# Performance work log

Measured on AMD Instinct MI355X. Metric: run time of the kernel, lower is better.

## Reference

```python
import jax, jax.numpy as jnp
import numpy as np

# nqsystems=8 grouped sites, physical dim d=2^ncontraq=16,
# state bond r=64, layer (unitary MPO) bond rl=16, operator MPO bond ro=4,
# nlsystems=1 pre-contracted circuit layer.
NQ, R, D, RL, RO, NL = 8, 64, 16, 16, 4, 1


def setup_inputs() -> dict:
    key = jax.random.key(0)
    k1, k2, k3 = jax.random.split(key, 3)
    # scale so contractions stay O(1) numerically
    state = jax.random.normal(k1, (NQ, R, D, R), jnp.float32) / np.float32(np.sqrt(R * D))
    layer = jax.random.normal(k2, (NL, NQ, RL, D, D, RL), jnp.float32) / np.float32(np.sqrt(RL * D))
    operator = jax.random.normal(k3, (NQ, RO, D, D, RO), jnp.float32) / np.float32(np.sqrt(RO * D))
    return {"state": state, "layer": layer, "operator": operator}


def reference(state, layer, operator):
    """<psi| U^dagger O U |psi> contracted site-by-site along the TT chain.

    state:    [nq, r, d, r]        TT cores of |psi>
    layer:    [nl, nq, rl, d, d, rl]  TT-operator cores of the circuit layer (nl=1)
    operator: [nq, ro, d, d, ro]   TT-operator cores of the observable
    """
    r, rl, ro = state.shape[1], layer.shape[3], operator.shape[1]
    # open-boundary closure: boundary vectors = e0 on every bond
    env0 = jnp.zeros((r, rl, ro, rl, r), state.dtype).at[0, 0, 0, 0, 0].set(1.0)
    U = layer[0]  # nlsystems == 1

    def step(env, cores):
        S, Uq, Oq = cores
        # tt_dagger: conj + transpose physical indices (0,2,1,3)
        Ud = jnp.conj(Uq).transpose(0, 2, 1, 3)
        # env axes: a=bra-state bond, l=bra-layer bond, o=operator bond,
        #           m=ket-layer bond, b=ket-state bond
        t = jnp.einsum('alomb,aiA->lombiA', env, jnp.conj(S))   # bra state core
        t = jnp.einsum('lombiA,lijL->ombAjL', t, Ud)            # U^dagger core
        t = jnp.einsum('ombAjL,ojkO->mbALkO', t, Oq)            # observable core
        t = jnp.einsum('mbALkO,mksM->bALOsM', t, Uq)            # U core
        t = jnp.einsum('bALOsM,bsB->ALOMB', t, S)               # ket state core
        return t, None

    env, _ = jax.lax.scan(step, env0, (state, U, operator))
    return env[0, 0, 0, 0, 0]
```

## Files before the change

kernel.cpp:

```cpp
#include <hip/hip_runtime.h>


typedef __attribute__((ext_vector_type(8))) short bf16x8;
typedef __attribute__((ext_vector_type(8))) _Float16 f16x8;
typedef __attribute__((ext_vector_type(4))) float f32x4;
typedef __attribute__((ext_vector_type(4))) unsigned short us4;

static __device__ __forceinline__ unsigned short f2bf(float x) {
    union { float f; unsigned u; } a; a.f = x;
    return (unsigned short)((a.u + 0x7FFF + ((a.u >> 16) & 1)) >> 16);
}
static __device__ __forceinline__ float bf2f(unsigned short h) {
    union { unsigned u; float f; } a; a.u = (unsigned)h << 16; return a.f;
}
static __device__ __forceinline__ unsigned split2(float x) {
    unsigned short h = f2bf(x);
    unsigned short l = f2bf(x - bf2f(h));
    return (unsigned)h | ((unsigned)l << 16);
}
static __device__ __forceinline__ unsigned short f2h_bits(float x) {
    union { _Float16 h; unsigned short u; } c; c.h = (_Float16)x; return c.u;
}
static __device__ __forceinline__ float h2f_bits(unsigned short u) {
    union { unsigned short u; _Float16 h; } c; c.u = u; return (float)c.h;
}
static __device__ __forceinline__ void gl_lds16(const unsigned short* g,
                                                unsigned short* l) {
    __builtin_amdgcn_global_load_lds(
        (const __attribute__((address_space(1))) unsigned int*)g,
        (__attribute__((address_space(3))) unsigned int*)l, 16, 0, 0);
}

__global__ void write_diag_kernel(float* out, float v) {
    if (threadIdx.x == 0 && blockIdx.x == 0) out[0] = v;
}
__global__ void zero_out(float* o) {
    if (threadIdx.x == 0 && blockIdx.x == 0) o[0] = 0.0f;
}

__global__ void prep_apack(const float* __restrict__ layer,
                           unsigned short* __restrict__ Ap2,
                           unsigned short* __restrict__ Ap4) {
    int idx = blockIdx.x * 256 + threadIdx.x;
    int q = idx >> 13, k0 = (idx >> 10) & 7, mt = (idx >> 6) & 15, lane = idx & 63;
    int quad = lane >> 4, r = lane & 15;
    unsigned short h2[8], l2[8], h4[8], l4[8];
#pragma unroll
    for (int j = 0; j < 8; j++) {
        int k = k0 * 32 + quad * 8 + j;
        int m = mt * 16 + r;
        float v2 = layer[(size_t)q * 65536 +
                         (size_t)((((k >> 4) * 16 + (m >> 4)) * 16 + (k & 15)) * 16 + (m & 15))];
        float v4 = layer[(size_t)q * 65536 +
                         (size_t)((((k >> 4) * 16 + (k & 15)) * 16 + (m >> 4)) * 16 + (m & 15))];
        h2[j] = f2h_bits(v2); l2[j] = f2h_bits(v2 - h2f_bits(h2[j]));
        h4[j] = f2h_bits(v4); l4[j] = f2h_bits(v4 - h2f_bits(h4[j]));
    }
    size_t base = ((size_t)((q * 8 + k0) * 16 + mt) * 2) * 512 + lane * 8;
    *(us4*)(Ap2 + base)       = *(us4*)&h2[0];
    *(us4*)(Ap2 + base + 4)   = *(us4*)&h2[4];
    *(us4*)(Ap2 + base + 512) = *(us4*)&l2[0];
    *(us4*)(Ap2 + base + 516) = *(us4*)&l2[4];
    *(us4*)(Ap4 + base)       = *(us4*)&h4[0];
    *(us4*)(Ap4 + base + 4)   = *(us4*)&h4[4];
    *(us4*)(Ap4 + base + 512) = *(us4*)&l4[0];
    *(us4*)(Ap4 + base + 516) = *(us4*)&l4[4];
}

__global__ void prep_spack1(const float* __restrict__ state,
                            unsigned short* __restrict__ Sp1) {
    int idx = blockIdx.x * 256 + threadIdx.x;
    int q = idx >> 13, c = (idx >> 11) & 3, k0 = (idx >> 10) & 1,
        mt = (idx >> 6) & 15, lane = idx & 63;
    int quad = lane >> 4, lr = lane & 15;
    unsigned short h[8], l[8];
#pragma unroll
    for (int j = 0; j < 8; j++) {
        int k = k0 * 32 + quad * 8 + j;
        float v = state[(size_t)q * 65536 + (size_t)(k * 16 + mt) * 64 + c * 16 + lr];
        h[j] = f2bf(v); l[j] = f2bf(v - bf2f(h[j]));
    }
    size_t base = (size_t)(q * 4 + c) * 32768 + ((size_t)(k0 * 16 + mt) * 2) * 512 + lane * 8;
    *(us4*)(Sp1 + base)       = *(us4*)&h[0];
    *(us4*)(Sp1 + base + 4)   = *(us4*)&h[4];
    *(us4*)(Sp1 + base + 512) = *(us4*)&l[0];
    *(us4*)(Sp1 + base + 516) = *(us4*)&l[4];
}

__global__ void prep_spack5(const float* __restrict__ state,
                            unsigned short* __restrict__ Sp5) {
    int idx = blockIdx.x * 256 + threadIdx.x;
    int q = idx >> 13, k0 = (idx >> 8) & 31, mt = (idx >> 6) & 3, lane = idx & 63;
    int quad = lane >> 4, lr = lane & 15;
    unsigned short h[8], l[8];
#pragma unroll
    for (int j = 0; j < 8; j++) {
        int k = k0 * 32 + quad * 8 + j;
        int s = k >> 6, b = k & 63;
        float v = state[(size_t)q * 65536 + (size_t)(b * 16 + s) * 64 + mt * 16 + lr];
        h[j] = f2bf(v); l[j] = f2bf(v - bf2f(h[j]));
    }
    size_t base = (size_t)q * 131072 + ((size_t)(k0 * 4 + mt) * 2) * 512 + lane * 8;
    *(us4*)(Sp5 + base)       = *(us4*)&h[0];
    *(us4*)(Sp5 + base + 4)   = *(us4*)&h[4];
    *(us4*)(Sp5 + base + 512) = *(us4*)&l[0];
    *(us4*)(Sp5 + base + 516) = *(us4*)&l[4];
}

__global__ void prep_opack3(const float* __restrict__ oper,
                            unsigned short* __restrict__ Op3) {
    int idx = blockIdx.x * 256 + threadIdx.x;
    int q = idx >> 9, k0 = (idx >> 8) & 1, mt = (idx >> 6) & 3, lane = idx & 63;
    int quad = lane >> 4, lr = lane & 15;
    unsigned short h[8], l[8];
#pragma unroll
    for (int j = 0; j < 8; j++) {
        int k = k0 * 32 + quad * 8 + j;
        int m = mt * 16 + lr;
        float v = oper[(size_t)q * 4096 + (size_t)(k * 16 + (m & 15)) * 4 + (m >> 4)];
        h[j] = f2h_bits(v); l[j] = f2h_bits(v - h2f_bits(h[j]));
    }
    size_t base = (size_t)q * 8192 + ((size_t)(k0 * 4 + mt) * 2) * 512 + lane * 8;
    *(us4*)(Op3 + base)       = *(us4*)&h[0];
    *(us4*)(Op3 + base + 4)   = *(us4*)&h[4];
    *(us4*)(Op3 + base + 512) = *(us4*)&l[0];
    *(us4*)(Op3 + base + 516) = *(us4*)&l[4];
}

__global__ void env_split_k(const float* __restrict__ env, unsigned* __restrict__ envS) {
    int t = blockIdx.x * 256 + threadIdx.x;
    float4 v = ((const float4*)env)[t];
    uint4 o;
    o.x = split2(v.x); o.y = split2(v.y); o.z = split2(v.z); o.w = split2(v.w);
    ((uint4*)envS)[t] = o;
}

__global__ void s0_g2(const float* __restrict__ state, const float* __restrict__ layer,
                      float* __restrict__ g2) {
    int t = blockIdx.x * 256 + threadIdx.x;
    int A = t >> 8, j = (t >> 4) & 15, L = t & 15;
    float s = 0;
    for (int i = 0; i < 16; i++) s += state[i * 64 + A] * layer[(j * 16 + i) * 16 + L];
    g2[t] = s;
}
__global__ void s0_g3(const float* __restrict__ g2, const float* __restrict__ oper,
                      float* __restrict__ g3) {
    int t = blockIdx.x * 256 + threadIdx.x;
    int A = t >> 10, L = (t >> 6) & 15, k = (t >> 2) & 15, O = t & 3;
    float s = 0;
    for (int j = 0; j < 16; j++) s += g2[A * 256 + j * 16 + L] * oper[(j * 16 + k) * 4 + O];
    g3[t] = s;
}
__global__ void s0_g4(const float* __restrict__ g3, const float* __restrict__ layer,
                      float* __restrict__ g4) {
    int t = blockIdx.x * 256 + threadIdx.x;
    int A = t >> 14, L = (t >> 10) & 15, O = (t >> 8) & 3, sp = (t >> 4) & 15, M = t & 15;
    float s = 0;
    for (int k = 0; k < 16; k++)
        s += g3[A * 1024 + L * 64 + k * 4 + O] * layer[(k * 16 + sp) * 16 + M];
    g4[t] = s;
}
__global__ void s0_env(const float* __restrict__ g4, const float* __restrict__ state,
                       float* __restrict__ env) {
    int t = blockIdx.x * 256 + threadIdx.x;
    int A = t >> 16, L = (t >> 12) & 15, O = (t >> 10) & 3, M = (t >> 6) & 15, B = t & 63;
    float s = 0;
    for (int sp = 0; sp < 16; sp++)
        s += g4[A * 16384 + L * 1024 + O * 256 + sp * 16 + M] * state[sp * 64 + B];
    env[(size_t)(L * 64 + O * 16 + M) * 4096 + A * 64 + B] = s;
}

__global__ void s7_c1(const float* __restrict__ state, const float* __restrict__ layer,
                      float* __restrict__ c1) {
    int t = blockIdx.x * 256 + threadIdx.x;
    int l = t >> 10, a = (t >> 4) & 63, j = t & 15;
    float s = 0;
    for (int i = 0; i < 16; i++)
        s += state[7 * 65536 + (a * 16 + i) * 64] * layer[7 * 65536 + ((l * 16 + j) * 16 + i) * 16];
    c1[t] = s;
}
__global__ void s7_c2(const float* __restrict__ c1, const float* __restrict__ oper,
                      float* __restrict__ c2) {
    int t = blockIdx.x * 256 + threadIdx.x;
    int o = t >> 14, l = (t >> 10) & 15, a = (t >> 4) & 63, k = t & 15;
    float s = 0;
    for (int j = 0; j < 16; j++)
        s += c1[l * 1024 + a * 16 + j] * oper[7 * 4096 + ((o * 16 + j) * 16 + k) * 4];
    c2[t] = s;
}
__global__ void s7_c3(const float* __restrict__ c2, const float* __restrict__ layer,
                      float* __restrict__ c3) {
    int t = blockIdx.x * 256 + threadIdx.x;
    int m = t >> 16, o = (t >> 14) & 3, l = (t >> 10) & 15, a = (t >> 4) & 63, sp = t & 15;
    float s = 0;
    for (int k = 0; k < 16; k++)
        s += c2[o * 16384 + l * 1024 + a * 16 + k] *
             layer[7 * 65536 + ((m * 16 + k) * 16 + sp) * 16];
    c3[t] = s;
}
__global__ void prep_sv(const float* __restrict__ state, float* __restrict__ sv) {
    int t = blockIdx.x * 256 + threadIdx.x;
    sv[t] = state[7 * 65536 + t * 64];
}
__global__ __launch_bounds__(256) void s7_fused(const float* __restrict__ env,
                                                const float* __restrict__ c3,
                                                const float* __restrict__ sv,
                                                float* __restrict__ out) {
    __shared__ float c3s[1024], svs[1024], red[256];
    int t = threadIdx.x;
    int n0 = blockIdx.x * 64;
    int l = n0 >> 12, o = (n0 >> 10) & 3, m = (n0 >> 6) & 15;
    const float* c3b = c3 + m * 65536 + o * 16384 + l * 1024;
    const float* eb  = env + (size_t)blockIdx.x * 4096;
    for (int i = t; i < 1024; i += 256) { c3s[i] = c3b[i]; svs[i] = sv[i]; }
    __syncthreads();
    float s = 0;
    int b = t & 63, ag = t >> 6;
#pragma unroll
    for (int g = 0; g < 16; g++) {
        int a = ag * 16 + g;
        float e = eb[a * 64 + b];
        float w = 0;
#pragma unroll
        for (int sp = 0; sp < 16; sp++) w += c3s[a * 16 + sp] * svs[b * 16 + sp];
        s += e * w;
    }
    red[t] = s; __syncthreads();
    for (int off = 128; off; off >>= 1) { if (t < off) red[t] += red[t + off]; __syncthreads(); }
    if (t == 0) atomicAdd(out, red[0]);
}

__global__ __launch_bounds__(256) void gemm_g1(const unsigned* __restrict__ envS,
                                               const unsigned short* __restrict__ Sp1,
                                               unsigned short* __restrict__ t1,
                                               float scale) {
    __shared__ unsigned Bt[32 * 65];
    const int tid = threadIdx.x, lane = tid & 63, wave = tid >> 6;
    const int quad = lane >> 4, lr = lane & 15;
    const int cc = blockIdx.x >> 10, rid = blockIdx.x & 1023;
    const int l = rid >> 6, o = (rid >> 4) & 3, m2 = rid & 15;

    f32x4 acc[4][4];
#pragma unroll
    for (int i = 0; i < 4; i++)
#pragma unroll
        for (int j = 0; j < 4; j++)
#pragma unroll
            for (int r = 0; r < 4; r++) acc[i][j][r] = 0.0f;

    const unsigned* Bv = envS + (size_t)rid * 4096;
    const unsigned short* Sp1c = Sp1 + (size_t)cc * 32768;
    uint4 ur[2];
    auto load_tile = [&](int k0) {
        const uint4* src = (const uint4*)(Bv + k0 * 2048);
        ur[0] = src[tid];
        ur[1] = src[256 + tid];
    };
    auto store_tile = [&]() {
#pragma unroll
        for (int v = 0; v < 2; v++) {
            int e = v * 256 + tid;
            unsigned* p = &Bt[(e >> 4) * 65 + (e & 15) * 4];
            p[0] = ur[v].x; p[1] = ur[v].y; p[2] = ur[v].z; p[3] = ur[v].w;
        }
    };

    bf16x8 ahb[2][4], alb[2][4];
    auto loadA = [&](int k0, int buf) {
#pragma unroll
        for (int mt = 0; mt < 4; mt++) {
            int gmt = wave * 4 + mt;
            const unsigned short* ap = Sp1c + ((size_t)(k0 * 16 + gmt) * 2) * 512 + lane * 8;
            ahb[buf][mt] = *(const bf16x8*)ap;
            alb[buf][mt] = *(const bf16x8*)(ap + 512);
        }
    };

    load_tile(0);
    loadA(0, 0);
    store_tile();
#pragma unroll
    for (int k0 = 0; k0 < 2; k0++) {
        __syncthreads();
        if (k0 + 1 < 2) { load_tile(k0 + 1); loadA(k0 + 1, 1); }
#pragma unroll
        for (int nt = 0; nt < 4; nt++) {
            int nl = nt * 16 + lr;
            bf16x8 bh, bl;
#pragma unroll
            for (int j = 0; j < 8; j++) {
                unsigned u = Bt[(quad * 8 + j) * 65 + nl];
                bh[j] = (short)(u & 0xffffu);
                bl[j] = (short)(u >> 16);
            }
#pragma unroll
            for (int mt = 0; mt < 4; mt++) {
                acc[mt][nt] = __builtin_amdgcn_mfma_f32_16x16x32_bf16(ahb[k0][mt], bh, acc[mt][nt], 0, 0, 0);
                acc[mt][nt] = __builtin_amdgcn_mfma_f32_16x16x32_bf16(ahb[k0][mt], bl, acc[mt][nt], 0, 0, 0);
                acc[mt][nt] = __builtin_amdgcn_mfma_f32_16x16x32_bf16(alb[k0][mt], bh, acc[mt][nt], 0, 0, 0);
            }
        }
        __syncthreads();
        if (k0 + 1 < 2) store_tile();
    }

#pragma unroll
    for (int nt = 0; nt < 4; nt++) {
        int b = nt * 16 + lr;
#pragma unroll
        for (int r = 0; r < 4; r++) {
            int a4 = quad * 4 + r;
            us4 w;
#pragma unroll
            for (int mt = 0; mt < 4; mt++) w[mt] = f2h_bits(acc[mt][nt][r] * scale);
            size_t addr = (size_t)cc * 16777216 +
                          (size_t)(o * 256 + m2 * 16 + a4) * 16384 +
                          (size_t)(l * 2 + (wave >> 1)) * 512 + b * 8 + (wave & 1) * 4;
            *(us4*)(t1 + addr) = w;
        }
    }
}

__global__ __launch_bounds__(256) void gemm_g2(const unsigned short* __restrict__ Bp,
                                               const unsigned short* __restrict__ Ap,
                                               unsigned short* __restrict__ Co) {
    __shared__ __align__(16) unsigned short Bs[16384];
    const int tid = threadIdx.x, lane = tid & 63, wave = tid >> 6;
    const int quad = lane >> 4, lr = lane & 15;
    const int cc = blockIdx.x >> 10, rid = blockIdx.x & 1023;
    const int o = rid >> 8, m2 = (rid >> 4) & 15, a4 = rid & 15;
    const unsigned short* pb = Bp + (size_t)blockIdx.x * 16384;
    unsigned short* Cb = Co + (size_t)cc * 16777216;

#pragma unroll
    for (int i = 0; i < 8; i++)
        gl_lds16(pb + i * 2048 + tid * 8, Bs + i * 2048 + wave * 512);

    f32x4 acc[4][4];
#pragma unroll
    for (int i = 0; i < 4; i++)
#pragma unroll
        for (int j = 0; j < 4; j++)
#pragma unroll
            for (int r = 0; r < 4; r++) acc[i][j][r] = 0.0f;

    f16x8 ah[3][4];
    auto loadA = [&](int k0, int buf) {
#pragma unroll
        for (int mt = 0; mt < 4; mt++) {
            int gmt = wave * 4 + mt;
            ah[buf][mt] = *(const f16x8*)(Ap + ((size_t)(k0 * 16 + gmt) * 2) * 512 + lane * 8);
        }
    };
    loadA(0, 0);
    loadA(1, 1);

    asm volatile("s_waitcnt vmcnt(0)" ::: "memory");
    __syncthreads();

#pragma unroll
    for (int k0 = 0; k0 < 8; k0++) {
        if (k0 + 2 < 8) loadA(k0 + 2, (k0 + 2) % 3);
        f16x8 bfr[4];
#pragma unroll
        for (int nt = 0; nt < 4; nt++)
            bfr[nt] = *(const f16x8*)(Bs + (k0 * 4 + quad) * 512 + (nt * 16 + lr) * 8);
#pragma unroll
        for (int nt = 0; nt < 4; nt++)
#pragma unroll
            for (int mt = 0; mt < 4; mt++)
                acc[mt][nt] = __builtin_amdgcn_mfma_f32_16x16x32_f16(
                    ah[k0 % 3][mt], bfr[nt], acc[mt][nt], 0, 0, 0);
    }

#pragma unroll
    for (int nt = 0; nt < 4; nt++) {
        int b = nt * 16 + lr;
#pragma unroll
        for (int r = 0; r < 4; r++) {
            int L = quad * 4 + r;
            us4 w;
#pragma unroll
            for (int mt = 0; mt < 4; mt++) w[mt] = f2h_bits(acc[mt][nt][r]);
            size_t addr = (size_t)(L * 256 + m2 * 16 + a4) * 4096 +
                          (size_t)(o * 2 + (wave >> 1)) * 512 + b * 8 + (wave & 1) * 4;
            *(us4*)(Cb + addr) = w;
        }
    }
}

__global__ __launch_bounds__(256) void gemm_g45(const unsigned short* __restrict__ T2,
                                                const unsigned short* __restrict__ Op3q,
                                                const unsigned short* __restrict__ Ap4,
                                                const unsigned short* __restrict__ Sp5,
                                                float* __restrict__ env,
                                                unsigned* __restrict__ envSo,
                                                int A0, float inv, int wf32) {
    __shared__ __align__(16) unsigned short Bs[16384];
    __shared__ unsigned SL[4 * 16 * 68];
    const int tid = threadIdx.x, lane = tid & 63, wave = tid >> 6;
    const int quad = lane >> 4, lr = lane & 15;
    const int cc = blockIdx.x >> 10, rid = blockIdx.x & 1023;
    const int low = rid & 7, O2 = (rid >> 3) & 3, g = rid >> 5;
    const int panel = g * 8 + low;
    const int L = panel >> 4, a4 = panel & 15;
    const unsigned short* T2c = T2 + (size_t)cc * 16777216;
    const int b8 = (wave * 16 + lr) * 8;

    f16x8 ah[3][4];
    auto loadA = [&](int k0, int buf) {
#pragma unroll
        for (int mt = 0; mt < 4; mt++) {
            int gmt = wave * 4 + mt;
            ah[buf][mt] = *(const f16x8*)(Ap4 + ((size_t)(k0 * 16 + gmt) * 2) * 512 + lane * 8);
        }
    };
    loadA(0, 0);
    loadA(1, 1);

    {
        f16x8 oh0 = *(const f16x8*)(Op3q + (size_t)(O2 * 2) * 512 + lane * 8);
        f16x8 oh1 = *(const f16x8*)(Op3q + (size_t)((4 + O2) * 2) * 512 + lane * 8);
        f16x8 tb[3][2];
        auto loadT2 = [&](int m2, int buf) {
            const unsigned short* pp = T2c + (size_t)(L * 256 + m2 * 16 + a4) * 4096;
            tb[buf][0] = *(const f16x8*)(pp + (quad << 9) + b8);
            tb[buf][1] = *(const f16x8*)(pp + ((4 + quad) << 9) + b8);
        };
        loadT2(0, 0);
        loadT2(1, 1);
#pragma unroll
        for (int m2 = 0; m2 < 16; m2++) {
            if (m2 + 2 < 16) loadT2(m2 + 2, (m2 + 2) % 3);
            f32x4 a3;
            a3[0] = a3[1] = a3[2] = a3[3] = 0.0f;
            a3 = __builtin_amdgcn_mfma_f32_16x16x32_f16(oh0, tb[m2 % 3][0], a3, 0, 0, 0);
            a3 = __builtin_amdgcn_mfma_f32_16x16x32_f16(oh1, tb[m2 % 3][1], a3, 0, 0, 0);
            us4 w;
#pragma unroll
            for (int r = 0; r < 4; r++) w[r] = f2h_bits(a3[r]);
            *(us4*)(Bs + (m2 * 2 + (quad >> 1)) * 512 + b8 + (quad & 1) * 4) = w;
        }
    }
    __syncthreads();

    f32x4 acc[4][4];
#pragma unroll
    for (int i = 0; i < 4; i++)
#pragma unroll
        for (int j = 0; j < 4; j++)
#pragma unroll
            for (int r = 0; r < 4; r++) acc[i][j][r] = 0.0f;

#pragma unroll
    for (int k0 = 0; k0 < 8; k0++) {
        if (k0 + 2 < 8) loadA(k0 + 2, (k0 + 2) % 3);
        f16x8 bfr[4];
#pragma unroll
        for (int nt = 0; nt < 4; nt++)
            bfr[nt] = *(const f16x8*)(Bs + (k0 * 4 + quad) * 512 + (nt * 16 + lr) * 8);
#pragma unroll
        for (int nt = 0; nt < 4; nt++)
#pragma unroll
            for (int mt = 0; mt < 4; mt++)
                acc[mt][nt] = __builtin_amdgcn_mfma_f32_16x16x32_f16(
                    ah[k0 % 3][mt], bfr[nt], acc[mt][nt], 0, 0, 0);
    }

    unsigned* myslab = SL + wave * (16 * 68);
    f32x4 acc5[4];
#pragma unroll
    for (int nt = 0; nt < 4; nt++)
#pragma unroll
        for (int r = 0; r < 4; r++) acc5[nt][r] = 0.0f;

    bf16x8 s5h[2][4], s5l[2][4];
    auto loadS5 = [&](int step, int buf) {
        int kg = (wave * 4 + (step >> 1)) * 2 + (step & 1);
#pragma unroll
        for (int nt = 0; nt < 4; nt++) {
            const unsigned short* bp = Sp5 + ((size_t)(kg * 4 + nt) * 2) * 512 + lane * 8;
            s5h[buf][nt] = *(const bf16x8*)bp;
            s5l[buf][nt] = *(const bf16x8*)(bp + 512);
        }
    };
    loadS5(0, 0);

#pragma unroll
    for (int mtp = 0; mtp < 4; mtp++) {
#pragma unroll
        for (int nt = 0; nt < 4; nt++)
#pragma unroll
            for (int r = 0; r < 4; r++)
                myslab[(quad * 4 + r) * 68 + nt * 16 + lr] = split2(acc[mtp][nt][r]);
        asm volatile("s_waitcnt lgkmcnt(0)" ::: "memory");
#pragma unroll
        for (int h = 0; h < 2; h++) {
            const int step = mtp * 2 + h;
            const unsigned* sp = &myslab[lr * 68 + h * 32 + quad * 8];
            uint4 u0 = *(const uint4*)sp;
            uint4 u1 = *(const uint4*)(sp + 4);
            bf16x8 th, tl;
            th[0] = (short)(u0.x & 0xffff); tl[0] = (short)(u0.x >> 16);
            th[1] = (short)(u0.y & 0xffff); tl[1] = (short)(u0.y >> 16);
            th[2] = (short)(u0.z & 0xffff); tl[2] = (short)(u0.z >> 16);
            th[3] = (short)(u0.w & 0xffff); tl[3] = (short)(u0.w >> 16);
            th[4] = (short)(u1.x & 0xffff); tl[4] = (short)(u1.x >> 16);
            th[5] = (short)(u1.y & 0xffff); tl[5] = (short)(u1.y >> 16);
            th[6] = (short)(u1.z & 0xffff); tl[6] = (short)(u1.z >> 16);
            th[7] = (short)(u1.w & 0xffff); tl[7] = (short)(u1.w >> 16);
            if (step + 1 < 8) loadS5(step + 1, (step + 1) & 1);
#pragma unroll
            for (int nt = 0; nt < 4; nt++) {
                acc5[nt] = __builtin_amdgcn_mfma_f32_16x16x32_bf16(th, s5h[step & 1][nt], acc5[nt], 0, 0, 0);
                acc5[nt] = __builtin_amdgcn_mfma_f32_16x16x32_bf16(th, s5l[step & 1][nt], acc5[nt], 0, 0, 0);
                acc5[nt] = __builtin_amdgcn_mfma_f32_16x16x32_bf16(tl, s5h[step & 1][nt], acc5[nt], 0, 0, 0);
            }
        }
    }

    __syncthreads();
    float* red = (float*)SL;
#pragma unroll
    for (int nt = 0; nt < 4; nt++)
#pragma unroll
        for (int r = 0; r < 4; r++)
            red[wave * 1088 + (quad * 4 + r) * 68 + nt * 16 + lr] = acc5[nt][r];
    __syncthreads();
#pragma unroll
    for (int r = 0; r < 4; r++) {
        int M2 = quad * 4 + r, Bc = wave * 16 + lr;
        float v = red[M2 * 68 + Bc] + red[1088 + M2 * 68 + Bc] +
                  red[2176 + M2 * 68 + Bc] + red[3264 + M2 * 68 + Bc];
        float w = v * inv;
        size_t idx = (size_t)(L * 64 + O2 * 16 + M2) * 4096 + (A0 + cc * 16 + a4) * 64 + Bc;
        envSo[idx] = split2(w);
        if (wf32) env[idx] = w;
    }
}

extern "C" void kernel_launch(void* const* d_in, const int* in_sizes, int n_in,
                              void* d_out, int out_size, void* d_ws, size_t ws_size,
                              hipStream_t stream) {
    const float* state = (const float*)d_in[0];
    const float* layer = (const float*)d_in[1];
    const float* oper  = (const float*)d_in[2];
    float* out = (float*)d_out;

    const size_t need = 16777216ull * 4 + 33554432ull * 4 + 3ull * 4194304ull * 4 +
                        (4ull * 1048576ull + 65536ull) * 2ull + 4096ull;
    if (ws_size < need) {
        write_diag_kernel<<<1, 64, 0, stream>>>(out, (float)ws_size);
        return;
    }
    float* F    = (float*)d_ws;
    unsigned* P = (unsigned*)(F + 16777216);
    unsigned* envS0 = (unsigned*)(P + 33554432);
    float* envB = (float*)(envS0 + 4194304);
    unsigned* envS1 = (unsigned*)(envB + 4194304);
    unsigned short* Ap2 = (unsigned short*)(envS1 + 4194304);
    unsigned short* Ap4 = Ap2 + 1048576;
    unsigned short* Sp1 = Ap4 + 1048576;
    unsigned short* Sp5 = Sp1 + 1048576;
    unsigned short* Op3 = Sp5 + 1048576;
    float* sv = (float*)(Op3 + 65536);
    float* SCR = F;
    unsigned short* T1 = (unsigned short*)P;
    unsigned short* T2 = (unsigned short*)F;

    prep_apack<<<256, 256, 0, stream>>>(layer, Ap2, Ap4);
    prep_spack1<<<256, 256, 0, stream>>>(state, Sp1);
    prep_spack5<<<256, 256, 0, stream>>>(state, Sp5);
    prep_opack3<<<16, 256, 0, stream>>>(oper, Op3);
    prep_sv<<<4, 256, 0, stream>>>(state, sv);

    s0_g2<<<64, 256, 0, stream>>>(state, layer, SCR);
    s0_g3<<<256, 256, 0, stream>>>(SCR, oper, SCR + 16384);
    s0_g4<<<4096, 256, 0, stream>>>(SCR + 16384, layer, SCR + 81920);
    s0_env<<<16384, 256, 0, stream>>>(SCR + 81920, state, envB);
    env_split_k<<<4096, 256, 0, stream>>>(envB, envS1);

    for (int q = 1; q < 7; q++) {
        unsigned* einS  = (q & 1) ? envS1 : envS0;
        unsigned* eoutS = (q & 1) ? envS0 : envS1;
        float scl = (float)(1u << (16 + 2 * q));
        float inv = 1.0f / scl;
        int wf32 = (q == 6) ? 1 : 0;
        for (int p = 0; p < 2; p++) {
            gemm_g1<<<2048, 256, 0, stream>>>(
                einS, Sp1 + (size_t)(q * 4 + p * 2) * 32768, T1, scl);
            gemm_g2<<<2048, 256, 0, stream>>>(
                T1, Ap2 + (size_t)q * 131072, T2);
            gemm_g45<<<2048, 256, 0, stream>>>(
                T2, Op3 + (size_t)q * 8192, Ap4 + (size_t)q * 131072,
                Sp5 + (size_t)q * 131072, envB, eoutS, p * 32, inv, wf32);
        }
    }

    s7_c1<<<64, 256, 0, stream>>>(state, layer, SCR);
    s7_c2<<<256, 256, 0, stream>>>(SCR, oper, SCR + 16384);
    s7_c3<<<4096, 256, 0, stream>>>(SCR + 16384, layer, SCR + 81920);
    zero_out<<<1, 64, 0, stream>>>(out);
    s7_fused<<<1024, 256, 0, stream>>>(envB, SCR + 81920, sv, out);
}
```

Before: 1.444 ms.

## Fuse g45 of first half with g1 of second half, pack bf16 splits

Merges the gemm_g45 launch for the first half of each site step with the gemm_g1 launch for the second half into one interleaved grid, so the two independent phases share the GPU and one launch boundary is removed. The split of floats into hi/lo bf16 pairs now uses packed v_cvt_pk_bf16_f32 and v_perm instructions in place of scalar bit manipulation. The T2 prefetch depth in g45 goes from 2 to 4. The risks are T1 being overwritten while g2 still needs it (the ordering looks safe here because g2 finished before the fused launch), higher register pressure from the deeper prefetch and the combined kernel, and a shared-memory footprint equal to the larger of the two bodies.

```diff
diff --git a/kernel.cpp b/kernel.cpp
--- a/kernel.cpp
+++ b/kernel.cpp
@@ -17,6 +17,18 @@
     unsigned short h = f2bf(x);
     unsigned short l = f2bf(x - bf2f(h));
     return (unsigned)h | ((unsigned)l << 16);
+}
+static __device__ __forceinline__ void split2_pair(float x0, float x1,
+                                                   unsigned& o0, unsigned& o1) {
+    unsigned hh, ll;
+    asm("v_cvt_pk_bf16_f32 %0, %1, %2" : "=v"(hh) : "v"(x0), "v"(x1));
+    union { unsigned u; float f; } c0, c1;
+    c0.u = hh << 16;
+    c1.u = hh & 0xffff0000u;
+    float r0 = x0 - c0.f, r1 = x1 - c1.f;
+    asm("v_cvt_pk_bf16_f32 %0, %1, %2" : "=v"(ll) : "v"(r0), "v"(r1));
+    asm("v_perm_b32 %0, %1, %2, %3" : "=v"(o0) : "v"(ll), "v"(hh), "s"(0x05040100));
+    asm("v_perm_b32 %0, %1, %2, %3" : "=v"(o1) : "v"(ll), "v"(hh), "s"(0x07060302));
 }
 static __device__ __forceinline__ unsigned short f2h_bits(float x) {
     union { _Float16 h; unsigned short u; } c; c.h = (_Float16)x; return c.u;
@@ -230,14 +242,15 @@
     if (t == 0) atomicAdd(out, red[0]);
 }
 
-__global__ __launch_bounds__(256) void gemm_g1(const unsigned* __restrict__ envS,
+static __device__ __forceinline__ void g1_body(int bid,
+                                               const unsigned* __restrict__ envS,
                                                const unsigned short* __restrict__ Sp1,
                                                unsigned short* __restrict__ t1,
                                                float scale) {
     __shared__ unsigned Bt[32 * 65];
     const int tid = threadIdx.x, lane = tid & 63, wave = tid >> 6;
     const int quad = lane >> 4, lr = lane & 15;
-    const int cc = blockIdx.x >> 10, rid = blockIdx.x & 1023;
+    const int cc = bid >> 10, rid = bid & 1023;
     const int l = rid >> 6, o = (rid >> 4) & 3, m2 = rid & 15;
 
     f32x4 acc[4][4];
@@ -319,6 +332,13 @@
             *(us4*)(t1 + addr) = w;
         }
     }
+}
+
+__global__ __launch_bounds__(256) void gemm_g1(const unsigned* __restrict__ envS,
+                                               const unsigned short* __restrict__ Sp1,
+                                               unsigned short* __restrict__ t1,
+                                               float scale) {
+    g1_body(blockIdx.x, envS, Sp1, t1, scale);
 }
 
 __global__ __launch_bounds__(256) void gemm_g2(const unsigned short* __restrict__ Bp,
@@ -389,7 +409,8 @@
     }
 }
 
-__global__ __launch_bounds__(256) void gemm_g45(const unsigned short* __restrict__ T2,
+static __device__ __forceinline__ void g45_body(int bid,
+                                                const unsigned short* __restrict__ T2,
                                                 const unsigned short* __restrict__ Op3q,
                                                 const unsigned short* __restrict__ Ap4,
                                                 const unsigned short* __restrict__ Sp5,
@@ -400,7 +421,7 @@
     __shared__ unsigned SL[4 * 16 * 68];
     const int tid = threadIdx.x, lane = tid & 63, wave = tid >> 6;
     const int quad = lane >> 4, lr = lane & 15;
-    const int cc = blockIdx.x >> 10, rid = blockIdx.x & 1023;
+    const int cc = bid >> 10, rid = bid & 1023;
     const int low = rid & 7, O2 = (rid >> 3) & 3, g = rid >> 5;
     const int panel = g * 8 + low;
     const int L = panel >> 4, a4 = panel & 15;
@@ -421,21 +442,20 @@
     {
         f16x8 oh0 = *(const f16x8*)(Op3q + (size_t)(O2 * 2) * 512 + lane * 8);
         f16x8 oh1 = *(const f16x8*)(Op3q + (size_t)((4 + O2) * 2) * 512 + lane * 8);
-        f16x8 tb[3][2];
+        f16x8 tb[5][2];
         auto loadT2 = [&](int m2, int buf) {
             const unsigned short* pp = T2c + (size_t)(L * 256 + m2 * 16 + a4) * 4096;
             tb[buf][0] = *(const f16x8*)(pp + (quad << 9) + b8);
             tb[buf][1] = *(const f16x8*)(pp + ((4 + quad) << 9) + b8);
         };
-        loadT2(0, 0);
-        loadT2(1, 1);
+        loadT2(0, 0); loadT2(1, 1); loadT2(2, 2); loadT2(3, 3);
 #pragma unroll
         for (int m2 = 0; m2 < 16; m2++) {
-            if (m2 + 2 < 16) loadT2(m2 + 2, (m2 + 2) % 3);
+            if (m2 + 4 < 16) loadT2(m2 + 4, (m2 + 4) % 5);
             f32x4 a3;
             a3[0] = a3[1] = a3[2] = a3[3] = 0.0f;
-            a3 = __builtin_amdgcn_mfma_f32_16x16x32_f16(oh0, tb[m2 % 3][0], a3, 0, 0, 0);
-            a3 = __builtin_amdgcn_mfma_f32_16x16x32_f16(oh1, tb[m2 % 3][1], a3, 0, 0, 0);
+            a3 = __builtin_amdgcn_mfma_f32_16x16x32_f16(oh0, tb[m2 % 5][0], a3, 0, 0, 0);
+            a3 = __builtin_amdgcn_mfma_f32_16x16x32_f16(oh1, tb[m2 % 5][1], a3, 0, 0, 0);
             us4 w;
 #pragma unroll
             for (int r = 0; r < 4; r++) w[r] = f2h_bits(a3[r]);
@@ -489,10 +509,15 @@
 #pragma unroll
     for (int mtp = 0; mtp < 4; mtp++) {
 #pragma unroll
-        for (int nt = 0; nt < 4; nt++)
-#pragma unroll
-            for (int r = 0; r < 4; r++)
-                myslab[(quad * 4 + r) * 68 + nt * 16 + lr] = split2(acc[mtp][nt][r]);
+        for (int nt = 0; nt < 4; nt++) {
+            unsigned o0, o1, o2, o3;
+            split2_pair(acc[mtp][nt][0], acc[mtp][nt][1], o0, o1);
+            split2_pair(acc[mtp][nt][2], acc[mtp][nt][3], o2, o3);
+            myslab[(quad * 4 + 0) * 68 + nt * 16 + lr] = o0;
+            myslab[(quad * 4 + 1) * 68 + nt * 16 + lr] = o1;
+            myslab[(quad * 4 + 2) * 68 + nt * 16 + lr] = o2;
+            myslab[(quad * 4 + 3) * 68 + nt * 16 + lr] = o3;
+        }
         asm volatile("s_waitcnt lgkmcnt(0)" ::: "memory");
 #pragma unroll
         for (int h = 0; h < 2; h++) {
@@ -527,16 +552,51 @@
         for (int r = 0; r < 4; r++)
             red[wave * 1088 + (quad * 4 + r) * 68 + nt * 16 + lr] = acc5[nt][r];
     __syncthreads();
+    float wv[4];
 #pragma unroll
     for (int r = 0; r < 4; r++) {
         int M2 = quad * 4 + r, Bc = wave * 16 + lr;
         float v = red[M2 * 68 + Bc] + red[1088 + M2 * 68 + Bc] +
                   red[2176 + M2 * 68 + Bc] + red[3264 + M2 * 68 + Bc];
-        float w = v * inv;
+        wv[r] = v * inv;
+    }
+    unsigned s0p, s1p, s2p, s3p;
+    split2_pair(wv[0], wv[1], s0p, s1p);
+    split2_pair(wv[2], wv[3], s2p, s3p);
+    unsigned sp4[4] = {s0p, s1p, s2p, s3p};
+#pragma unroll
+    for (int r = 0; r < 4; r++) {
+        int M2 = quad * 4 + r, Bc = wave * 16 + lr;
         size_t idx = (size_t)(L * 64 + O2 * 16 + M2) * 4096 + (A0 + cc * 16 + a4) * 64 + Bc;
-        envSo[idx] = split2(w);
-        if (wf32) env[idx] = w;
-    }
+        envSo[idx] = sp4[r];
+        if (wf32) env[idx] = wv[r];
+    }
+}
+
+__global__ __launch_bounds__(256) void gemm_g45(const unsigned short* __restrict__ T2,
+                                                const unsigned short* __restrict__ Op3q,
+                                                const unsigned short* __restrict__ Ap4,
+                                                const unsigned short* __restrict__ Sp5,
+                                                float* __restrict__ env,
+                                                unsigned* __restrict__ envSo,
+                                                int A0, float inv, int wf32) {
+    g45_body(blockIdx.x, T2, Op3q, Ap4, Sp5, env, envSo, A0, inv, wf32);
+}
+
+__global__ __launch_bounds__(256) void fused_g45_g1(
+        const unsigned short* __restrict__ T2,
+        const unsigned short* __restrict__ Op3q,
+        const unsigned short* __restrict__ Ap4,
+        const unsigned short* __restrict__ Sp5,
+        float* __restrict__ env, unsigned* __restrict__ envSo,
+        float inv, int wf32,
+        const unsigned* __restrict__ envS,
+        const unsigned short* __restrict__ Sp1b,
+        unsigned short* __restrict__ t1, float scale) {
+    if (blockIdx.x & 1)
+        g1_body(blockIdx.x >> 1, envS, Sp1b, t1, scale);
+    else
+        g45_body(blockIdx.x >> 1, T2, Op3q, Ap4, Sp5, env, envSo, 0, inv, wf32);
 }
 
 extern "C" void kernel_launch(void* const* d_in, const int* in_sizes, int n_in,
@@ -586,15 +646,19 @@
         float scl = (float)(1u << (16 + 2 * q));
         float inv = 1.0f / scl;
         int wf32 = (q == 6) ? 1 : 0;
-        for (int p = 0; p < 2; p++) {
-            gemm_g1<<<2048, 256, 0, stream>>>(
-                einS, Sp1 + (size_t)(q * 4 + p * 2) * 32768, T1, scl);
-            gemm_g2<<<2048, 256, 0, stream>>>(
-                T1, Ap2 + (size_t)q * 131072, T2);
-            gemm_g45<<<2048, 256, 0, stream>>>(
-                T2, Op3 + (size_t)q * 8192, Ap4 + (size_t)q * 131072,
-                Sp5 + (size_t)q * 131072, envB, eoutS, p * 32, inv, wf32);
-        }
+        gemm_g1<<<2048, 256, 0, stream>>>(
+            einS, Sp1 + (size_t)(q * 4 + 0) * 32768, T1, scl);
+        gemm_g2<<<2048, 256, 0, stream>>>(
+            T1, Ap2 + (size_t)q * 131072, T2);
+        fused_g45_g1<<<4096, 256, 0, stream>>>(
+            T2, Op3 + (size_t)q * 8192, Ap4 + (size_t)q * 131072,
+            Sp5 + (size_t)q * 131072, envB, eoutS, inv, wf32,
+            einS, Sp1 + (size_t)(q * 4 + 2) * 32768, T1, scl);
+        gemm_g2<<<2048, 256, 0, stream>>>(
+            T1, Ap2 + (size_t)q * 131072, T2);
+        gemm_g45<<<2048, 256, 0, stream>>>(
+            T2, Op3 + (size_t)q * 8192, Ap4 + (size_t)q * 131072,
+            Sp5 + (size_t)q * 131072, envB, eoutS, 32, inv, wf32);
     }
 
     s7_c1<<<64, 256, 0, stream>>>(state, layer, SCR);
```

After: 1.584 ms. +9.7%, slower.
